# Optimization experiments

Hardware: AMD Instinct MI355X
Metric: run time of the kernel (lower is better)

Reference implementation:

```python
import jax, jax.numpy as jnp
import numpy as np

K = 3  # kernel size from init_kwargs


def setup_inputs() -> dict:
    key = jax.random.key(0)
    x = jax.random.normal(key, (16, K * K, 512, 512), dtype=jnp.float32)
    return {"x": x}


def reference(x) -> jnp.ndarray:
    # Faithful col2im / fold: conv_transpose2d with identity-channel weight,
    # stride=1, padding=K//2. Channel c = i*K + j contributes tap (i,j):
    #   out[b, p, q] = sum_{i,j} x[b, i*K+j, p - (i - pad), q - (j - pad)]
    # Implemented as 9 static shifted-slice adds (no wasted zero multiplies).
    k = K
    pad = k // 2
    b, c, h, w = x.shape
    xp = jnp.pad(x, ((0, 0), (0, 0), (pad, pad), (pad, pad)))  # [b, k^2, h+2p, w+2p]
    out = jnp.zeros((b, h, w), dtype=x.dtype)
    for i in range(k):
        for j in range(k):
            ch = i * k + j
            ri = 2 * pad - i  # row slice start
            cj = 2 * pad - j  # col slice start
            out = out + xp[:, ch, ri:ri + h, cj:cj + w]
    return out[:, None, :, :]  # [b, 1, h, w]
```

## Files before the change

kernel.cpp:

```cpp
#include <hip/hip_runtime.h>


constexpr int B = 16;
constexpr int C = 9;
constexpr int H = 512;
constexpr int W = 512;
constexpr int WV = W / 4;

typedef float f4_u __attribute__((ext_vector_type(4), aligned(4)));

__global__ __launch_bounds__(256) void fold_kernel(const float* __restrict__ x,
                                                   float* __restrict__ out) {
    const int tid = blockIdx.x * blockDim.x + threadIdx.x;
    const int qv = tid % WV;
    const int t2 = tid / WV;
    const int p  = t2 % H;
    const int b  = t2 / H;
    const int q0 = qv * 4;

    const size_t plane = (size_t)H * W;
    const float* xb = x + (size_t)b * C * plane;

    float ax = 0.f, ay = 0.f, az = 0.f, aw = 0.f;
    const bool interior = (qv != 0) & (qv != WV - 1);

#pragma unroll
    for (int i = 0; i < 3; ++i) {
        const int r = p + 1 - i;
        if (r < 0 || r >= H) continue;
#pragma unroll
        for (int j = 0; j < 3; ++j) {
            const float* xrow = xb + (size_t)(i * 3 + j) * plane + (size_t)r * W;
            const int c0 = q0 + 1 - j;
            if (interior) {
                f4_u v = *reinterpret_cast<const f4_u*>(xrow + c0);
                ax += v.x; ay += v.y; az += v.z; aw += v.w;
            } else {
                if (c0 >= 0 && c0 < W)         ax += xrow[c0];
                if (c0 + 1 >= 0 && c0 + 1 < W) ay += xrow[c0 + 1];
                if (c0 + 2 >= 0 && c0 + 2 < W) az += xrow[c0 + 2];
                if (c0 + 3 >= 0 && c0 + 3 < W) aw += xrow[c0 + 3];
            }
        }
    }

    f4_u r;
    r.x = ax; r.y = ay; r.z = az; r.w = aw;
    *reinterpret_cast<f4_u*>(out + (size_t)tid * 4) = r;
}

extern "C" void kernel_launch(void* const* d_in, const int* in_sizes, int n_in,
                              void* d_out, int out_size, void* d_ws, size_t ws_size,
                              hipStream_t stream) {
    const float* x = (const float*)d_in[0];
    float* out = (float*)d_out;
    const int n_threads = B * H * WV;
    const int block = 256;
    const int grid = n_threads / block;
    fold_kernel<<<grid, block, 0, stream>>>(x, out);
}
```

Before: 209.0 us.

## Use aligned float4 loads with wavefront shuffles for horizontal shifts

Each thread now issues only aligned 16-byte loads at q0 for each channel row and sums the three vertical taps per column offset into three vector accumulators. The one-column horizontal shifts are recovered with cross-lane shuffles, and only the edge lanes of each wavefront issue a scalar load for the missing neighbour. This removes the unaligned vector loads and the scalar boundary path. The output is written with nontemporal stores and index math uses shifts and masks. It relies on wavefront size 64 and on a row segment mapping contiguously to lanes.

After: 211.7 us. Within noise of the previous version (+1.3%).

```diff
diff --git a/kernel.cpp b/kernel.cpp
--- a/kernel.cpp
+++ b/kernel.cpp
@@ -7,46 +7,57 @@
 constexpr int W = 512;
 constexpr int WV = W / 4;
 
-typedef float f4_u __attribute__((ext_vector_type(4), aligned(4)));
+typedef float f4 __attribute__((ext_vector_type(4)));
 
 __global__ __launch_bounds__(256) void fold_kernel(const float* __restrict__ x,
                                                    float* __restrict__ out) {
     const int tid = blockIdx.x * blockDim.x + threadIdx.x;
-    const int qv = tid % WV;
-    const int t2 = tid / WV;
-    const int p  = t2 % H;
-    const int b  = t2 / H;
+    const int qv = tid & (WV - 1);
+    const int t2 = tid >> 7;
+    const int p  = t2 & (H - 1);
+    const int b  = t2 >> 9;
     const int q0 = qv * 4;
+    const int lane = threadIdx.x & 63;
 
     const size_t plane = (size_t)H * W;
     const float* xb = x + (size_t)b * C * plane;
 
-    float ax = 0.f, ay = 0.f, az = 0.f, aw = 0.f;
-    const bool interior = (qv != 0) & (qv != WV - 1);
+    f4 A  = {0.f, 0.f, 0.f, 0.f};
+    f4 Bv = {0.f, 0.f, 0.f, 0.f};
+    f4 Cv = {0.f, 0.f, 0.f, 0.f};
+    float aR = 0.f, cL = 0.f;
+
+    const bool needR = (lane == 63) && (q0 + 4 < W);
+    const bool needL = (lane == 0) && (q0 > 0);
 
 #pragma unroll
     for (int i = 0; i < 3; ++i) {
         const int r = p + 1 - i;
         if (r < 0 || r >= H) continue;
-#pragma unroll
-        for (int j = 0; j < 3; ++j) {
-            const float* xrow = xb + (size_t)(i * 3 + j) * plane + (size_t)r * W;
-            const int c0 = q0 + 1 - j;
-            if (interior) {
-                f4_u v = *reinterpret_cast<const f4_u*>(xrow + c0);
-                ax += v.x; ay += v.y; az += v.z; aw += v.w;
-            } else {
-                if (c0 >= 0 && c0 < W)         ax += xrow[c0];
-                if (c0 + 1 >= 0 && c0 + 1 < W) ay += xrow[c0 + 1];
-                if (c0 + 2 >= 0 && c0 + 2 < W) az += xrow[c0 + 2];
-                if (c0 + 3 >= 0 && c0 + 3 < W) aw += xrow[c0 + 3];
-            }
-        }
+        const float* r0 = xb + (size_t)(3 * i + 0) * plane + (size_t)r * W;
+        const float* r1 = xb + (size_t)(3 * i + 1) * plane + (size_t)r * W;
+        const float* r2 = xb + (size_t)(3 * i + 2) * plane + (size_t)r * W;
+
+        A  += *reinterpret_cast<const f4*>(r0 + q0);
+        Bv += *reinterpret_cast<const f4*>(r1 + q0);
+        Cv += *reinterpret_cast<const f4*>(r2 + q0);
+
+        if (needR) aR += r0[q0 + 4];
+        if (needL) cL += r2[q0 - 1];
     }
 
-    f4_u r;
-    r.x = ax; r.y = ay; r.z = az; r.w = aw;
-    *reinterpret_cast<f4_u*>(out + (size_t)tid * 4) = r;
+    float a_next = __shfl_down(A.x, 1, 64);
+    if (lane == 63) a_next = aR;
+    float c_prev = __shfl_up(Cv.w, 1, 64);
+    if (lane == 0) c_prev = cL;
+
+    f4 o;
+    o.x = A.y    + Bv.x + c_prev;
+    o.y = A.z    + Bv.y + Cv.x;
+    o.z = A.w    + Bv.z + Cv.y;
+    o.w = a_next + Bv.w + Cv.z;
+
+    __builtin_nontemporal_store(o, reinterpret_cast<f4*>(out + (size_t)tid * 4));
 }
 
 extern "C" void kernel_launch(void* const* d_in, const int* in_sizes, int n_in,
```
